# Optimization experiments

Measured on AMD Instinct MI355X. Metric: run time of the kernel, lower is better.

The kernel has to match this reference:

```python
import jax, jax.numpy as jnp
import numpy as np

IC, HC, L, T, BS = 512, 512, 2, 512, 64
FORGET_BIAS = 1.0


def setup_inputs() -> dict:
    key = jax.random.key(0)
    k_x, k0, k1 = jax.random.split(key, 3)
    # xavier_normal std = sqrt(2/(fan_in+fan_out)), bias zeros (per module init)
    std0 = float(np.sqrt(2.0 / ((IC + HC) + 4 * HC)))
    std1 = float(np.sqrt(2.0 / ((HC + HC) + 4 * HC)))
    return {
        "x": jax.random.normal(k_x, (T, BS, IC), dtype=jnp.float32),
        "W0": jax.random.normal(k0, (IC + HC, 4 * HC), dtype=jnp.float32) * std0,
        "b0": jnp.zeros((4 * HC,), dtype=jnp.float32),
        "W1": jax.random.normal(k1, (HC + HC, 4 * HC), dtype=jnp.float32) * std1,
        "b1": jnp.zeros((4 * HC,), dtype=jnp.float32),
        "h0": jnp.zeros((L, 1, HC), dtype=jnp.float32),
        "c0": jnp.zeros((L, 1, HC), dtype=jnp.float32),
    }


def _run_layer(W, b, x_seq, h_init, c_init):
    def step(carry, xt):
        h, c = carry
        z = jnp.concatenate([xt, h], axis=1) @ W + b  # [bs, 4*hc]
        f, i, o, g = jnp.split(z, 4, axis=1)
        f = jax.nn.sigmoid(f + FORGET_BIAS)
        i = jax.nn.sigmoid(i)
        o = jax.nn.sigmoid(o)
        g = jnp.tanh(g)
        c = c * f + g * i
        h = o * jnp.tanh(c)
        return (h, c), h

    (hT, cT), hs = jax.lax.scan(step, (h_init, c_init), x_seq)
    return hs, hT, cT


def reference(x, W0, b0, W1, b1, h0, c0):
    bs = x.shape[1]
    h = jnp.broadcast_to(h0, (L, bs, HC))
    c = jnp.broadcast_to(c0, (L, bs, HC))
    params = [(W0, b0), (W1, b1)]
    lstm_input = x
    hs_final, cs_final = [], []
    for layer in range(L):
        W, b = params[layer]
        lstm_input, hT, cT = _run_layer(W, b, lstm_input, h[layer], c[layer])
        hs_final.append(hT)
        cs_final.append(cT)
    out = lstm_input  # [T, bs, hc]
    hs = jnp.stack(hs_final, axis=0)  # [L, bs, hc]
    cs = jnp.stack(cs_final, axis=0)
    return (out, (hs, cs))
```

## Files before the change

### kernel.cpp

```cpp
#include <hip/hip_runtime.h>
#include <cstdint>
#include <cstddef>


#define T_STEPS 512
#define WROW 1032

typedef float f32x4 __attribute__((ext_vector_type(4)));
typedef short s16x8 __attribute__((ext_vector_type(8)));

__device__ __forceinline__ unsigned short f2bf(float f) {
    unsigned int u = __builtin_bit_cast(unsigned int, f);
    u += 0x7FFFu + ((u >> 16) & 1u);
    return (unsigned short)(u >> 16);
}
__device__ __forceinline__ float sig_(float x)  { return 1.0f / (1.0f + __expf(-x)); }
__device__ __forceinline__ float tanh_(float x) { return 1.0f - 2.0f / (__expf(2.0f * x) + 1.0f); }

__device__ __forceinline__ s16x8 ldc(const unsigned short* p) {
    unsigned long long lo = __hip_atomic_load((unsigned long long*)p,     __ATOMIC_RELAXED, __HIP_MEMORY_SCOPE_AGENT);
    unsigned long long hi = __hip_atomic_load((unsigned long long*)p + 1, __ATOMIC_RELAXED, __HIP_MEMORY_SCOPE_AGENT);
    ulonglong2 u; u.x = lo; u.y = hi;
    return __builtin_bit_cast(s16x8, u);
}
__device__ __forceinline__ void stc(unsigned short* p, s16x8 v) {
    ulonglong2 u = __builtin_bit_cast(ulonglong2, v);
    __hip_atomic_store((unsigned long long*)p,     u.x, __ATOMIC_RELAXED, __HIP_MEMORY_SCOPE_AGENT);
    __hip_atomic_store((unsigned long long*)p + 1, u.y, __ATOMIC_RELAXED, __HIP_MEMORY_SCOPE_AGENT);
}


__global__ void k_conv_bf16(const float* __restrict__ src, unsigned short* __restrict__ dst) {
    int i = (blockIdx.x * 256 + threadIdx.x) * 8;
    float4 a = *(const float4*)(src + i);
    float4 b = *(const float4*)(src + i + 4);
    s16x8 o;
    o[0]=(short)f2bf(a.x); o[1]=(short)f2bf(a.y); o[2]=(short)f2bf(a.z); o[3]=(short)f2bf(a.w);
    o[4]=(short)f2bf(b.x); o[5]=(short)f2bf(b.y); o[6]=(short)f2bf(b.z); o[7]=(short)f2bf(b.w);
    *(s16x8*)(dst + i) = o;
}

__global__ void k_transpose_w(const float* __restrict__ W0, const float* __restrict__ W1,
                              unsigned short* __restrict__ WT0, unsigned short* __restrict__ WT1) {
    __shared__ unsigned short tile[32][33];
    const float* W = blockIdx.z ? W1 : W0;
    unsigned short* WT = blockIdx.z ? WT1 : WT0;
    int n0 = blockIdx.x * 32, k0 = blockIdx.y * 32;
    int tx = threadIdx.x, ty = threadIdx.y;
    #pragma unroll
    for (int i = 0; i < 4; i++)
        tile[ty + i*8][tx] = f2bf(W[(size_t)(k0 + ty + i*8) * 2048 + n0 + tx]);
    __syncthreads();
    #pragma unroll
    for (int i = 0; i < 4; i++)
        WT[(size_t)(n0 + ty + i*8) * 1024 + k0 + tx] = tile[tx][ty + i*8];
}

__global__ void k_hinit(const float* __restrict__ h0, unsigned short* __restrict__ hi0,
                        unsigned short* __restrict__ hi1) {
    int idx = blockIdx.x * 256 + threadIdx.x;
    int layer = idx >> 15;
    int r = idx & 32767;
    int b = r >> 9;
    int j = r & 511;
    unsigned short v = f2bf(h0[layer * 512 + j]);
    unsigned short* d = layer ? hi1 : hi0;
    d[(size_t)((j >> 3) * 64 + b) * 8 + (j & 7)] = v;
}

__global__ __launch_bounds__(256, 1) void k_lstm_fused(
    const unsigned short* __restrict__ xb,
    const unsigned short* __restrict__ hi0, const unsigned short* __restrict__ hi1,
    const unsigned short* __restrict__ WT0, const unsigned short* __restrict__ WT1,
    const float* __restrict__ b0, const float* __restrict__ b1,
    const float* __restrict__ c0,
    unsigned short* __restrict__ h0s, unsigned short* __restrict__ h1s,
    float* __restrict__ out, float* __restrict__ hs, float* __restrict__ cs,
    unsigned int* __restrict__ cnt)
{
    __shared__ unsigned short Wl[32][WROW];
    __shared__ unsigned short hstage[64][8];

    const int isl1 = (int)(blockIdx.x >> 6);
    const int wg   = (int)(blockIdx.x & 63);
    const int tid  = threadIdx.x;
    const int j0   = wg * 8;

    const unsigned short* WT    = isl1 ? WT1 : WT0;
    const float*          bias  = isl1 ? b1  : b0;
    const float*          c0l   = c0 + isl1 * 512;
    const unsigned short* hinit = isl1 ? hi1 : hi0;
    unsigned short*       hseq  = isl1 ? h1s : h0s;
    unsigned int* my_cnt   = cnt + isl1 * 64;
    unsigned int* prod_cnt = cnt;

    #pragma unroll
    for (int it = 0; it < 16; it++) {
        int idx = it * 256 + tid;
        int row = idx >> 7;
        int ch  = idx & 127;
        int cc_ = row & 15;
        int gate = (row >> 4) * 2 + (cc_ >> 3);
        int gr = gate * 512 + j0 + (cc_ & 7);
        *(s16x8*)(&Wl[row][ch * 8]) = *(const s16x8*)(WT + (size_t)gr * 1024 + ch * 8);
    }
    __syncthreads();

    const int lane = tid & 63;
    const int wv = tid >> 6;
    const int q = lane >> 4;
    const int cc = lane & 15;
    const int arow = wv * 16 + cc;
    const int jj = j0 + (cc & 7);
    const int bb = wv * 16 + q * 4;

    const float bias0 = (cc < 8) ? bias[jj] : bias[512 + jj];
    const float bias1 = (cc < 8) ? bias[1024 + jj] : bias[1536 + jj];
    float cst[4];
    {
        float ci = c0l[jj];
        cst[0] = cst[1] = cst[2] = cst[3] = ci;
    }

    for (int t = 0; t < T_STEPS; t++) {
        s16x8 af[32];
        if (!isl1) {
            const unsigned short* xp = xb + (size_t)(t * 64 + arow) * 512 + q * 8;
            #pragma unroll
            for (int kk = 0; kk < 16; kk++)
                af[kk] = *(const s16x8*)(xp + kk * 32);
        }

        if (isl1) {
            if (tid < 4) {
                unsigned int tgt = 16u * (unsigned int)(t + 1);
                while (__hip_atomic_load(prod_cnt + tid * 16, __ATOMIC_RELAXED, __HIP_MEMORY_SCOPE_AGENT) < tgt)
                    __builtin_amdgcn_s_sleep(1);
                if (t > 0) {
                    unsigned int tgt2 = 16u * (unsigned int)t;
                    while (__hip_atomic_load(my_cnt + tid * 16, __ATOMIC_RELAXED, __HIP_MEMORY_SCOPE_AGENT) < tgt2)
                        __builtin_amdgcn_s_sleep(1);
                }
            }
            __syncthreads();
        } else if (t > 0) {
            if (tid < 4) {
                unsigned int tgt = 16u * (unsigned int)t;
                while (__hip_atomic_load(my_cnt + tid * 16, __ATOMIC_RELAXED, __HIP_MEMORY_SCOPE_AGENT) < tgt)
                    __builtin_amdgcn_s_sleep(1);
            }
            __syncthreads();
        }

        if (isl1) {
            const unsigned short* xp = h0s + (size_t)t * 32768;
            #pragma unroll
            for (int kk = 0; kk < 16; kk++)
                af[kk] = ldc(xp + ((size_t)(kk * 4 + q) * 64 + arow) * 8);
        }
        {
            const unsigned short* hb = t ? (hseq + (size_t)(t - 1) * 32768) : hinit;
            #pragma unroll
            for (int kk = 0; kk < 16; kk++)
                af[16 + kk] = ldc(hb + ((size_t)(kk * 4 + q) * 64 + arow) * 8);
        }

        f32x4 acc0  = {bias0, bias0, bias0, bias0};
        f32x4 acc1  = {bias1, bias1, bias1, bias1};
        f32x4 acc0b = {0.f, 0.f, 0.f, 0.f};
        f32x4 acc1b = {0.f, 0.f, 0.f, 0.f};
        #pragma unroll
        for (int kk = 0; kk < 32; kk += 2) {
            s16x8 w00 = *(const s16x8*)(&Wl[cc][kk * 32 + q * 8]);
            s16x8 w10 = *(const s16x8*)(&Wl[16 + cc][kk * 32 + q * 8]);
            acc0  = __builtin_amdgcn_mfma_f32_16x16x32_bf16(af[kk], w00, acc0, 0, 0, 0);
            acc1  = __builtin_amdgcn_mfma_f32_16x16x32_bf16(af[kk], w10, acc1, 0, 0, 0);
            s16x8 w01 = *(const s16x8*)(&Wl[cc][(kk + 1) * 32 + q * 8]);
            s16x8 w11 = *(const s16x8*)(&Wl[16 + cc][(kk + 1) * 32 + q * 8]);
            acc0b = __builtin_amdgcn_mfma_f32_16x16x32_bf16(af[kk + 1], w01, acc0b, 0, 0, 0);
            acc1b = __builtin_amdgcn_mfma_f32_16x16x32_bf16(af[kk + 1], w11, acc1b, 0, 0, 0);
        }
        acc0 = acc0 + acc0b;
        acc1 = acc1 + acc1b;

        #pragma unroll
        for (int r = 0; r < 4; r++) {
            float z0 = acc0[r], z1 = acc1[r];
            float p0 = __shfl_xor(z0, 8, 64);
            float p1 = __shfl_xor(z1, 8, 64);
            float zf = (cc < 8) ? z0 : p0;
            float zi = (cc < 8) ? p0 : z0;
            float zo = (cc < 8) ? z1 : p1;
            float zg = (cc < 8) ? p1 : z1;
            float fg = sig_(zf + 1.0f);
            float ig = sig_(zi);
            float og = sig_(zo);
            float gg = tanh_(zg);
            float cn = cst[r] * fg + gg * ig;
            cst[r] = cn;
            float hv = og * tanh_(cn);
            int b = bb + r;
            if (cc < 8)
                hstage[b][cc] = f2bf(hv);
            if (isl1 && cc >= 8)
                out[(size_t)(t * 64 + b) * 512 + jj] = hv;
            if (t == T_STEPS - 1) {
                if (cc < 8) hs[(size_t)(isl1 * 64 + b) * 512 + jj] = hv;
                else        cs[(size_t)(isl1 * 64 + b) * 512 + jj] = cn;
            }
        }

        {
            unsigned short* hdst = hseq + (size_t)t * 32768 + (size_t)wg * 512;
            if (lane < 16) {
                int row = wv * 16 + lane;
                s16x8 v = *(const s16x8*)(&hstage[row][0]);
                stc(hdst + (size_t)row * 8, v);
            }
        }

        __syncthreads();
        if (tid == 0)
            __hip_atomic_fetch_add(my_cnt + (wg & 3) * 16, 1u, __ATOMIC_RELAXED, __HIP_MEMORY_SCOPE_AGENT);
    }
}


extern "C" void kernel_launch(void* const* d_in, const int* in_sizes, int n_in,
                              void* d_out, int out_size, void* d_ws, size_t ws_size,
                              hipStream_t stream) {
    const float* x  = (const float*)d_in[0];
    const float* W0 = (const float*)d_in[1];
    const float* b0 = (const float*)d_in[2];
    const float* W1 = (const float*)d_in[3];
    const float* b1 = (const float*)d_in[4];
    const float* h0 = (const float*)d_in[5];
    const float* c0 = (const float*)d_in[6];
    float* out = (float*)d_out;

    char* ws = (char*)d_ws;
    unsigned short* xb  = (unsigned short*)(ws);
    unsigned short* h0s = (unsigned short*)(ws + 33554432);
    unsigned short* h1s = (unsigned short*)(ws + 2 * 33554432);
    unsigned short* WT0 = (unsigned short*)(ws + 3 * 33554432);
    unsigned short* WT1 = (unsigned short*)(ws + 3 * 33554432 + 4194304);
    unsigned short* hi0 = (unsigned short*)(ws + 3 * 33554432 + 2 * 4194304);
    unsigned short* hi1 = (unsigned short*)(ws + 3 * 33554432 + 2 * 4194304 + 65536);
    unsigned int*   cnt = (unsigned int*)(ws + 3 * 33554432 + 2 * 4194304 + 2 * 65536);

    hipMemsetAsync(cnt, 0, 1024, stream);
    k_conv_bf16<<<8192, 256, 0, stream>>>(x, xb);
    k_transpose_w<<<dim3(64, 32, 2), dim3(32, 8), 0, stream>>>(W0, W1, WT0, WT1);
    k_hinit<<<256, 256, 0, stream>>>(h0, hi0, hi1);

    float* hs = out + 16777216;
    float* cs = hs + 65536;
    k_lstm_fused<<<128, 256, 0, stream>>>(xb, hi0, hi1, WT0, WT1, b0, b1, c0,
                                          h0s, h1s, out, hs, cs, cnt);
}
```

Baseline: 2.887 ms.

## Wavefront-fuse both LSTM layers per block with per-block step flags

Each of 64 blocks now holds the weight slices for both layers in shared memory. In skewed step tau it computes layer 0 at time tau and layer 1 at time tau-1, so the two layers share one grid-wide barrier per step instead of 128 blocks syncing through two counter groups. The barrier becomes per-block monotonic flags polled by one wave with ballot, replacing the atomic fetch-add counters and the producer/consumer waits. The trade-off is half as many blocks, each doing twice the MFMA work per step, and double the LDS footprint.

```diff
diff --git a/kernel.cpp b/kernel.cpp
--- a/kernel.cpp
+++ b/kernel.cpp
@@ -68,7 +68,7 @@
     d[(size_t)((j >> 3) * 64 + b) * 8 + (j & 7)] = v;
 }
 
-__global__ __launch_bounds__(256, 1) void k_lstm_fused(
+__global__ __launch_bounds__(256, 1) void k_lstm_fused2(
     const unsigned short* __restrict__ xb,
     const unsigned short* __restrict__ hi0, const unsigned short* __restrict__ hi1,
     const unsigned short* __restrict__ WT0, const unsigned short* __restrict__ WT1,
@@ -76,152 +76,205 @@
     const float* __restrict__ c0,
     unsigned short* __restrict__ h0s, unsigned short* __restrict__ h1s,
     float* __restrict__ out, float* __restrict__ hs, float* __restrict__ cs,
-    unsigned int* __restrict__ cnt)
+    unsigned int* __restrict__ flags)
 {
-    __shared__ unsigned short Wl[32][WROW];
-    __shared__ unsigned short hstage[64][8];
-
-    const int isl1 = (int)(blockIdx.x >> 6);
-    const int wg   = (int)(blockIdx.x & 63);
-    const int tid  = threadIdx.x;
-    const int j0   = wg * 8;
-
-    const unsigned short* WT    = isl1 ? WT1 : WT0;
-    const float*          bias  = isl1 ? b1  : b0;
-    const float*          c0l   = c0 + isl1 * 512;
-    const unsigned short* hinit = isl1 ? hi1 : hi0;
-    unsigned short*       hseq  = isl1 ? h1s : h0s;
-    unsigned int* my_cnt   = cnt + isl1 * 64;
-    unsigned int* prod_cnt = cnt;
+    __shared__ unsigned short Wl[2][32][WROW];
+    __shared__ unsigned short hst[2][64][8];
+
+    const int wg  = (int)blockIdx.x;
+    const int tid = (int)threadIdx.x;
+    const int j0  = wg * 8;
 
     #pragma unroll
-    for (int it = 0; it < 16; it++) {
-        int idx = it * 256 + tid;
-        int row = idx >> 7;
-        int ch  = idx & 127;
-        int cc_ = row & 15;
-        int gate = (row >> 4) * 2 + (cc_ >> 3);
-        int gr = gate * 512 + j0 + (cc_ & 7);
-        *(s16x8*)(&Wl[row][ch * 8]) = *(const s16x8*)(WT + (size_t)gr * 1024 + ch * 8);
+    for (int l = 0; l < 2; l++) {
+        const unsigned short* WT = l ? WT1 : WT0;
+        #pragma unroll
+        for (int it = 0; it < 16; it++) {
+            int idx = it * 256 + tid;
+            int row = idx >> 7;
+            int ch  = idx & 127;
+            int gate = (row >> 4) * 2 + ((row & 15) >> 3);
+            int gr = gate * 512 + j0 + (row & 7);
+            *(s16x8*)(&Wl[l][row][ch * 8]) = *(const s16x8*)(WT + (size_t)gr * 1024 + ch * 8);
+        }
     }
     __syncthreads();
 
     const int lane = tid & 63;
-    const int wv = tid >> 6;
-    const int q = lane >> 4;
-    const int cc = lane & 15;
+    const int wv   = tid >> 6;
+    const int q    = lane >> 4;
+    const int cc   = lane & 15;
     const int arow = wv * 16 + cc;
-    const int jj = j0 + (cc & 7);
-    const int bb = wv * 16 + q * 4;
-
-    const float bias0 = (cc < 8) ? bias[jj] : bias[512 + jj];
-    const float bias1 = (cc < 8) ? bias[1024 + jj] : bias[1536 + jj];
-    float cst[4];
-    {
-        float ci = c0l[jj];
-        cst[0] = cst[1] = cst[2] = cst[3] = ci;
-    }
-
-    for (int t = 0; t < T_STEPS; t++) {
-        s16x8 af[32];
-        if (!isl1) {
-            const unsigned short* xp = xb + (size_t)(t * 64 + arow) * 512 + q * 8;
+    const int jj   = j0 + (cc & 7);
+    const int bb   = wv * 16 + q * 4;
+
+    const float b0t0 = (cc < 8) ? b0[jj] : b0[512 + jj];
+    const float b0t1 = (cc < 8) ? b0[1024 + jj] : b0[1536 + jj];
+    const float b1t0 = (cc < 8) ? b1[jj] : b1[512 + jj];
+    const float b1t1 = (cc < 8) ? b1[1024 + jj] : b1[1536 + jj];
+    float cst0[4], cst1[4];
+    { float ci = c0[jj];       cst0[0]=cst0[1]=cst0[2]=cst0[3]=ci; }
+    { float ci = c0[512 + jj]; cst1[0]=cst1[1]=cst1[2]=cst1[3]=ci; }
+
+    for (int tau = 0; tau <= T_STEPS; tau++) {
+        s16x8 ax[16];
+        if (tau < T_STEPS) {
+            const unsigned short* xp = xb + (size_t)(tau * 64 + arow) * 512 + q * 8;
             #pragma unroll
             for (int kk = 0; kk < 16; kk++)
-                af[kk] = *(const s16x8*)(xp + kk * 32);
-        }
-
-        if (isl1) {
-            if (tid < 4) {
-                unsigned int tgt = 16u * (unsigned int)(t + 1);
-                while (__hip_atomic_load(prod_cnt + tid * 16, __ATOMIC_RELAXED, __HIP_MEMORY_SCOPE_AGENT) < tgt)
-                    __builtin_amdgcn_s_sleep(1);
-                if (t > 0) {
-                    unsigned int tgt2 = 16u * (unsigned int)t;
-                    while (__hip_atomic_load(my_cnt + tid * 16, __ATOMIC_RELAXED, __HIP_MEMORY_SCOPE_AGENT) < tgt2)
-                        __builtin_amdgcn_s_sleep(1);
+                ax[kk] = *(const s16x8*)(xp + kk * 32);
+        }
+
+        if (tau > 0) {
+            unsigned int tgt = (unsigned int)tau;
+            while (true) {
+                unsigned int v = __hip_atomic_load(flags + lane * 32, __ATOMIC_RELAXED, __HIP_MEMORY_SCOPE_AGENT);
+                if (__ballot(v < tgt) == 0ull) break;
+                __builtin_amdgcn_s_sleep(1);
+            }
+        }
+
+        s16x8 ah0[16];
+        {
+            const unsigned short* hb = tau ? (h0s + (size_t)(tau - 1) * 32768) : hi0;
+            #pragma unroll
+            for (int kk = 0; kk < 16; kk++)
+                ah0[kk] = ldc(hb + ((size_t)(kk * 4 + q) * 64 + arow) * 8);
+        }
+        s16x8 ah1[16];
+        if (tau > 0) {
+            const unsigned short* hb = (tau > 1) ? (h1s + (size_t)(tau - 2) * 32768) : hi1;
+            #pragma unroll
+            for (int kk = 0; kk < 16; kk++)
+                ah1[kk] = ldc(hb + ((size_t)(kk * 4 + q) * 64 + arow) * 8);
+        }
+
+        if (tau < T_STEPS) {
+            f32x4 a0  = {b0t0, b0t0, b0t0, b0t0};
+            f32x4 a1  = {b0t1, b0t1, b0t1, b0t1};
+            f32x4 a0b = {0.f, 0.f, 0.f, 0.f};
+            f32x4 a1b = {0.f, 0.f, 0.f, 0.f};
+            #pragma unroll
+            for (int kk = 0; kk < 16; kk += 2) {
+                s16x8 w00 = *(const s16x8*)(&Wl[0][cc][kk * 32 + q * 8]);
+                s16x8 w10 = *(const s16x8*)(&Wl[0][16 + cc][kk * 32 + q * 8]);
+                a0  = __builtin_amdgcn_mfma_f32_16x16x32_bf16(ax[kk], w00, a0, 0, 0, 0);
+                a1  = __builtin_amdgcn_mfma_f32_16x16x32_bf16(ax[kk], w10, a1, 0, 0, 0);
+                s16x8 w01 = *(const s16x8*)(&Wl[0][cc][(kk + 1) * 32 + q * 8]);
+                s16x8 w11 = *(const s16x8*)(&Wl[0][16 + cc][(kk + 1) * 32 + q * 8]);
+                a0b = __builtin_amdgcn_mfma_f32_16x16x32_bf16(ax[kk + 1], w01, a0b, 0, 0, 0);
+                a1b = __builtin_amdgcn_mfma_f32_16x16x32_bf16(ax[kk + 1], w11, a1b, 0, 0, 0);
+            }
+            #pragma unroll
+            for (int kk = 0; kk < 16; kk += 2) {
+                s16x8 w00 = *(const s16x8*)(&Wl[0][cc][(16 + kk) * 32 + q * 8]);
+                s16x8 w10 = *(const s16x8*)(&Wl[0][16 + cc][(16 + kk) * 32 + q * 8]);
+                a0  = __builtin_amdgcn_mfma_f32_16x16x32_bf16(ah0[kk], w00, a0, 0, 0, 0);
+                a1  = __builtin_amdgcn_mfma_f32_16x16x32_bf16(ah0[kk], w10, a1, 0, 0, 0);
+                s16x8 w01 = *(const s16x8*)(&Wl[0][cc][(17 + kk) * 32 + q * 8]);
+                s16x8 w11 = *(const s16x8*)(&Wl[0][16 + cc][(17 + kk) * 32 + q * 8]);
+                a0b = __builtin_amdgcn_mfma_f32_16x16x32_bf16(ah0[kk + 1], w01, a0b, 0, 0, 0);
+                a1b = __builtin_amdgcn_mfma_f32_16x16x32_bf16(ah0[kk + 1], w11, a1b, 0, 0, 0);
+            }
+            a0 = a0 + a0b;
+            a1 = a1 + a1b;
+
+            #pragma unroll
+            for (int r = 0; r < 4; r++) {
+                float z0 = a0[r], z1 = a1[r];
+                float p0 = __shfl_xor(z0, 8, 64);
+                float p1 = __shfl_xor(z1, 8, 64);
+                float zf = (cc < 8) ? z0 : p0;
+                float zi = (cc < 8) ? p0 : z0;
+                float zo = (cc < 8) ? z1 : p1;
+                float zg = (cc < 8) ? p1 : z1;
+                float fg = sig_(zf + 1.0f);
+                float ig = sig_(zi);
+                float og = sig_(zo);
+                float gg = tanh_(zg);
+                float cn = cst0[r] * fg + gg * ig;
+                cst0[r] = cn;
+                float hv = og * tanh_(cn);
+                int b = bb + r;
+                if (cc < 8) hst[0][b][cc] = f2bf(hv);
+                if (tau == T_STEPS - 1) {
+                    if (cc < 8) hs[(size_t)b * 512 + jj] = hv;
+                    else        cs[(size_t)b * 512 + jj] = cn;
                 }
             }
-            __syncthreads();
-        } else if (t > 0) {
-            if (tid < 4) {
-                unsigned int tgt = 16u * (unsigned int)t;
-                while (__hip_atomic_load(my_cnt + tid * 16, __ATOMIC_RELAXED, __HIP_MEMORY_SCOPE_AGENT) < tgt)
-                    __builtin_amdgcn_s_sleep(1);
-            }
-            __syncthreads();
-        }
-
-        if (isl1) {
-            const unsigned short* xp = h0s + (size_t)t * 32768;
-            #pragma unroll
-            for (int kk = 0; kk < 16; kk++)
-                af[kk] = ldc(xp + ((size_t)(kk * 4 + q) * 64 + arow) * 8);
-        }
-        {
-            const unsigned short* hb = t ? (hseq + (size_t)(t - 1) * 32768) : hinit;
-            #pragma unroll
-            for (int kk = 0; kk < 16; kk++)
-                af[16 + kk] = ldc(hb + ((size_t)(kk * 4 + q) * 64 + arow) * 8);
-        }
-
-        f32x4 acc0  = {bias0, bias0, bias0, bias0};
-        f32x4 acc1  = {bias1, bias1, bias1, bias1};
-        f32x4 acc0b = {0.f, 0.f, 0.f, 0.f};
-        f32x4 acc1b = {0.f, 0.f, 0.f, 0.f};
-        #pragma unroll
-        for (int kk = 0; kk < 32; kk += 2) {
-            s16x8 w00 = *(const s16x8*)(&Wl[cc][kk * 32 + q * 8]);
-            s16x8 w10 = *(const s16x8*)(&Wl[16 + cc][kk * 32 + q * 8]);
-            acc0  = __builtin_amdgcn_mfma_f32_16x16x32_bf16(af[kk], w00, acc0, 0, 0, 0);
-            acc1  = __builtin_amdgcn_mfma_f32_16x16x32_bf16(af[kk], w10, acc1, 0, 0, 0);
-            s16x8 w01 = *(const s16x8*)(&Wl[cc][(kk + 1) * 32 + q * 8]);
-            s16x8 w11 = *(const s16x8*)(&Wl[16 + cc][(kk + 1) * 32 + q * 8]);
-            acc0b = __builtin_amdgcn_mfma_f32_16x16x32_bf16(af[kk + 1], w01, acc0b, 0, 0, 0);
-            acc1b = __builtin_amdgcn_mfma_f32_16x16x32_bf16(af[kk + 1], w11, acc1b, 0, 0, 0);
-        }
-        acc0 = acc0 + acc0b;
-        acc1 = acc1 + acc1b;
-
-        #pragma unroll
-        for (int r = 0; r < 4; r++) {
-            float z0 = acc0[r], z1 = acc1[r];
-            float p0 = __shfl_xor(z0, 8, 64);
-            float p1 = __shfl_xor(z1, 8, 64);
-            float zf = (cc < 8) ? z0 : p0;
-            float zi = (cc < 8) ? p0 : z0;
-            float zo = (cc < 8) ? z1 : p1;
-            float zg = (cc < 8) ? p1 : z1;
-            float fg = sig_(zf + 1.0f);
-            float ig = sig_(zi);
-            float og = sig_(zo);
-            float gg = tanh_(zg);
-            float cn = cst[r] * fg + gg * ig;
-            cst[r] = cn;
-            float hv = og * tanh_(cn);
-            int b = bb + r;
-            if (cc < 8)
-                hstage[b][cc] = f2bf(hv);
-            if (isl1 && cc >= 8)
-                out[(size_t)(t * 64 + b) * 512 + jj] = hv;
-            if (t == T_STEPS - 1) {
-                if (cc < 8) hs[(size_t)(isl1 * 64 + b) * 512 + jj] = hv;
-                else        cs[(size_t)(isl1 * 64 + b) * 512 + jj] = cn;
-            }
-        }
-
-        {
-            unsigned short* hdst = hseq + (size_t)t * 32768 + (size_t)wg * 512;
-            if (lane < 16) {
-                int row = wv * 16 + lane;
-                s16x8 v = *(const s16x8*)(&hstage[row][0]);
-                stc(hdst + (size_t)row * 8, v);
-            }
+        }
+
+        if (tau > 0) {
+            const int t1 = tau - 1;
+            f32x4 a0  = {b1t0, b1t0, b1t0, b1t0};
+            f32x4 a1  = {b1t1, b1t1, b1t1, b1t1};
+            f32x4 a0b = {0.f, 0.f, 0.f, 0.f};
+            f32x4 a1b = {0.f, 0.f, 0.f, 0.f};
+            #pragma unroll
+            for (int kk = 0; kk < 16; kk += 2) {
+                s16x8 w00 = *(const s16x8*)(&Wl[1][cc][kk * 32 + q * 8]);
+                s16x8 w10 = *(const s16x8*)(&Wl[1][16 + cc][kk * 32 + q * 8]);
+                a0  = __builtin_amdgcn_mfma_f32_16x16x32_bf16(ah0[kk], w00, a0, 0, 0, 0);
+                a1  = __builtin_amdgcn_mfma_f32_16x16x32_bf16(ah0[kk], w10, a1, 0, 0, 0);
+                s16x8 w01 = *(const s16x8*)(&Wl[1][cc][(kk + 1) * 32 + q * 8]);
+                s16x8 w11 = *(const s16x8*)(&Wl[1][16 + cc][(kk + 1) * 32 + q * 8]);
+                a0b = __builtin_amdgcn_mfma_f32_16x16x32_bf16(ah0[kk + 1], w01, a0b, 0, 0, 0);
+                a1b = __builtin_amdgcn_mfma_f32_16x16x32_bf16(ah0[kk + 1], w11, a1b, 0, 0, 0);
+            }
+            #pragma unroll
+            for (int kk = 0; kk < 16; kk += 2) {
+                s16x8 w00 = *(const s16x8*)(&Wl[1][cc][(16 + kk) * 32 + q * 8]);
+                s16x8 w10 = *(const s16x8*)(&Wl[1][16 + cc][(16 + kk) * 32 + q * 8]);
+                a0  = __builtin_amdgcn_mfma_f32_16x16x32_bf16(ah1[kk], w00, a0, 0, 0, 0);
+                a1  = __builtin_amdgcn_mfma_f32_16x16x32_bf16(ah1[kk], w10, a1, 0, 0, 0);
+                s16x8 w01 = *(const s16x8*)(&Wl[1][cc][(17 + kk) * 32 + q * 8]);
+                s16x8 w11 = *(const s16x8*)(&Wl[1][16 + cc][(17 + kk) * 32 + q * 8]);
+                a0b = __builtin_amdgcn_mfma_f32_16x16x32_bf16(ah1[kk + 1], w01, a0b, 0, 0, 0);
+                a1b = __builtin_amdgcn_mfma_f32_16x16x32_bf16(ah1[kk + 1], w11, a1b, 0, 0, 0);
+            }
+            a0 = a0 + a0b;
+            a1 = a1 + a1b;
+
+            #pragma unroll
+            for (int r = 0; r < 4; r++) {
+                float z0 = a0[r], z1 = a1[r];
+                float p0 = __shfl_xor(z0, 8, 64);
+                float p1 = __shfl_xor(z1, 8, 64);
+                float zf = (cc < 8) ? z0 : p0;
+                float zi = (cc < 8) ? p0 : z0;
+                float zo = (cc < 8) ? z1 : p1;
+                float zg = (cc < 8) ? p1 : z1;
+                float fg = sig_(zf + 1.0f);
+                float ig = sig_(zi);
+                float og = sig_(zo);
+                float gg = tanh_(zg);
+                float cn = cst1[r] * fg + gg * ig;
+                cst1[r] = cn;
+                float hv = og * tanh_(cn);
+                int b = bb + r;
+                if (cc < 8) hst[1][b][cc] = f2bf(hv);
+                if (cc >= 8) out[(size_t)(t1 * 64 + b) * 512 + jj] = hv;
+                if (t1 == T_STEPS - 1) {
+                    if (cc < 8) hs[(size_t)(64 + b) * 512 + jj] = hv;
+                    else        cs[(size_t)(64 + b) * 512 + jj] = cn;
+                }
+            }
+        }
+
+        if (lane < 16) {
+            int row = wv * 16 + lane;
+            if (tau < T_STEPS)
+                stc(h0s + (size_t)tau * 32768 + (size_t)wg * 512 + (size_t)row * 8,
+                    *(const s16x8*)(&hst[0][row][0]));
+            if (tau > 0)
+                stc(h1s + (size_t)(tau - 1) * 32768 + (size_t)wg * 512 + (size_t)row * 8,
+                    *(const s16x8*)(&hst[1][row][0]));
         }
 
         __syncthreads();
-        if (tid == 0)
-            __hip_atomic_fetch_add(my_cnt + (wg & 3) * 16, 1u, __ATOMIC_RELAXED, __HIP_MEMORY_SCOPE_AGENT);
+        if (tid == 0 && tau < T_STEPS)
+            __hip_atomic_store(flags + wg * 32, (unsigned int)(tau + 1),
+                               __ATOMIC_RELAXED, __HIP_MEMORY_SCOPE_AGENT);
     }
 }
 
@@ -246,15 +299,15 @@
     unsigned short* WT1 = (unsigned short*)(ws + 3 * 33554432 + 4194304);
     unsigned short* hi0 = (unsigned short*)(ws + 3 * 33554432 + 2 * 4194304);
     unsigned short* hi1 = (unsigned short*)(ws + 3 * 33554432 + 2 * 4194304 + 65536);
-    unsigned int*   cnt = (unsigned int*)(ws + 3 * 33554432 + 2 * 4194304 + 2 * 65536);
-
-    hipMemsetAsync(cnt, 0, 1024, stream);
+    unsigned int*   flags = (unsigned int*)(ws + 3 * 33554432 + 2 * 4194304 + 2 * 65536);
+
+    hipMemsetAsync(flags, 0, 8192, stream);
     k_conv_bf16<<<8192, 256, 0, stream>>>(x, xb);
     k_transpose_w<<<dim3(64, 32, 2), dim3(32, 8), 0, stream>>>(W0, W1, WT0, WT1);
     k_hinit<<<256, 256, 0, stream>>>(h0, hi0, hi1);
 
     float* hs = out + 16777216;
     float* cs = hs + 65536;
-    k_lstm_fused<<<128, 256, 0, stream>>>(xb, hi0, hi1, WT0, WT1, b0, b1, c0,
-                                          h0s, h1s, out, hs, cs, cnt);
-}
+    k_lstm_fused2<<<64, 256, 0, stream>>>(xb, hi0, hi1, WT0, WT1, b0, b1, c0,
+                                          h0s, h1s, out, hs, cs, flags);
+}
```

Result: slower. 4.451 ms (+54.2%).
